# Performance work log

Hardware: AMD Instinct MI355X
Metric: run time of the kernel (lower is better)

## Reference

```python
import jax, jax.numpy as jnp
import numpy as np

K = 5
BN_EPS = 1e-5


def _knn(xyz1, xyz2, embedding_lens):
    # squared pairwise distances [B, N, S]
    d2 = (jnp.sum(xyz1 ** 2, -1)[:, :, None]
          + jnp.sum(xyz2 ** 2, -1)[:, None, :]
          - 2.0 * jnp.einsum('bnc,bsc->bns', xyz1, xyz2))
    S = xyz2.shape[1]
    valid2 = jnp.arange(S)[None, :] < embedding_lens[:, None]  # [B, S]
    d2 = jnp.where(valid2[:, None, :], d2, jnp.float32(1e10))
    neg, idx = jax.lax.top_k(-d2, K)  # K smallest distances
    return -neg, idx  # squared dists [B,N,K], indices [B,N,K]


def _masked_bn(x, mask_f, gamma, beta):
    # x: [B, N, C]; mask_f: [B, N, 1] float; stats over valid positions only
    cnt = jnp.sum(mask_f)
    mean = jnp.sum(x * mask_f, axis=(0, 1)) / cnt
    var = jnp.sum(((x - mean) ** 2) * mask_f, axis=(0, 1)) / cnt
    return (x - mean) * jax.lax.rsqrt(var + BN_EPS) * gamma + beta


def setup_inputs() -> dict:
    key = jax.random.key(0)
    ks = jax.random.split(key, 8)
    B, N, S, D1, D2 = 16, 2048, 512, 384, 384
    xyz1 = jax.random.normal(ks[0], (B, N, 3), jnp.float32)
    xyz2 = jax.random.normal(ks[1], (B, S, 3), jnp.float32)
    points1 = jax.random.normal(ks[2], (B, N, D1), jnp.float32)
    points2 = jax.random.normal(ks[3], (B, S, D2), jnp.float32)
    point_lens = jax.random.randint(ks[4], (B,), N // 2, N + 1).astype(jnp.int32)
    embedding_lens = jax.random.randint(ks[5], (B,), S // 2, S + 1).astype(jnp.int32)
    point_mask = jnp.arange(N)[None, :] < point_lens[:, None]  # [B, N] bool
    Cin = D1 + D2
    W0 = jax.random.normal(ks[6], (768, Cin), jnp.float32) * (1.0 / np.sqrt(Cin))
    W1 = jax.random.normal(ks[7], (384, 768), jnp.float32) * (1.0 / np.sqrt(768))
    return dict(xyz1=xyz1, xyz2=xyz2, points1=points1, points2=points2,
                point_lens=point_lens, embedding_lens=embedding_lens,
                point_mask=point_mask,
                W0=W0, g0=jnp.ones((768,), jnp.float32), b0=jnp.zeros((768,), jnp.float32),
                W1=W1, g1=jnp.ones((384,), jnp.float32), b1=jnp.zeros((384,), jnp.float32))


def reference(xyz1, xyz2, points1, points2, point_lens, embedding_lens,
              point_mask, W0, g0, b0, W1, g1, b1):
    B, N, _ = xyz1.shape
    D2 = points2.shape[-1]
    dists, idx = _knn(xyz1[..., :3], xyz2, embedding_lens)
    eps = jnp.finfo(dists.dtype).eps
    dist_recip = 1.0 / (dists + eps)                    # [B, N, K]
    weight = dist_recip / jnp.sum(dist_recip, axis=2, keepdims=True)
    # masked gather: points2[b, idx[b,n,k], :] -> [B, N, K, D2]
    gathered = jnp.take_along_axis(points2, idx.reshape(B, N * K)[..., None],
                                   axis=1).reshape(B, N, K, D2)
    interp = jnp.sum(gathered * weight[..., None], axis=2)  # [B, N, D2]
    x = jnp.concatenate([points1, interp], axis=-1)          # [B, N, D1+D2]
    mask_f = point_mask.astype(x.dtype)[..., None]           # [B, N, 1]
    for W, g, b in ((W0, g0, b0), (W1, g1, b1)):
        x = jnp.einsum('bnc,dc->bnd', x, W)  # 1x1 conv, no bias
        x = jax.nn.relu(_masked_bn(x, mask_f, g, b))
    return x
```

## Files before the change

### kernel.cpp

```cpp
#include <hip/hip_runtime.h>
#include <cstdint>
#include <cstddef>

typedef unsigned short u16;
typedef __bf16 bf16x8 __attribute__((ext_vector_type(8)));
typedef float    f32x4 __attribute__((ext_vector_type(4)));
typedef unsigned int u32x4 __attribute__((ext_vector_type(4)));

constexpr int BB   = 16;
constexpr int NN   = 2048;
constexpr int SS   = 512;
constexpr int DD   = 384;
constexpr int CIN  = 768;
constexpr int HID  = 768;
constexpr int OUTC = 384;
constexpr int MROWS = BB * NN;
constexpr float KNN_EPS = 1.1920929e-07f;
constexpr float BN_EPS  = 1e-5f;

constexpr size_t OFF_W0B  = 0;
constexpr size_t OFF_W1B  = OFF_W0B  + (size_t)HID*CIN*2;
constexpr size_t OFF_IDX  = OFF_W1B  + (size_t)OUTC*HID*2;
constexpr size_t OFF_WGT  = OFF_IDX  + (size_t)MROWS*5*4;
constexpr size_t OFF_SUM1 = OFF_WGT  + (size_t)MROWS*5*4;
constexpr size_t OFF_SUM2 = OFF_SUM1 + (size_t)HID*2*4;
constexpr size_t OFF_COEF1= OFF_SUM2 + (size_t)OUTC*2*4;
constexpr size_t OFF_COEF2= OFF_COEF1+ (size_t)HID*2*4;
constexpr size_t OFF_XCAT = OFF_COEF2+ (size_t)OUTC*2*4;
constexpr size_t OFF_H1   = OFF_XCAT + (size_t)MROWS*CIN*2;

__device__ inline float bf2f(u16 u){ unsigned int i = ((unsigned int)u)<<16; float f; __builtin_memcpy(&f,&i,4); return f; }
__device__ inline u16 f2bf(float f){ unsigned int x; __builtin_memcpy(&x,&f,4);
  unsigned int r = (x + 0x7fffu + ((x>>16)&1u)) >> 16; return (u16)r; }

__device__ inline void async16(const void* g, void* l){
  __builtin_amdgcn_global_load_lds((const __attribute__((address_space(1))) void*)g,
                                   (__attribute__((address_space(3))) void*)l, 16, 0, 0);
}

__global__ void cvtw_kernel(const float* __restrict__ W0, const float* __restrict__ W1,
                            u16* __restrict__ W0b, u16* __restrict__ W1b){
  int t = blockIdx.x*256 + threadIdx.x;
  if (t < HID*CIN)  W0b[t] = f2bf(W0[t]);
  if (t < OUTC*HID) W1b[t] = f2bf(W1[t]);
}

__global__ __launch_bounds__(256) void knn_kernel(const float* __restrict__ xyz1,
                                                  const float* __restrict__ xyz2,
                                                  const int* __restrict__ elens,
                                                  int* __restrict__ idxO, float* __restrict__ wO){
  __shared__ f32x4 sp[SS];
  const int tid = threadIdx.x;
  const int wv = tid >> 6, lane = tid & 63;
  const int wg = blockIdx.x*4 + wv;
  const int b = wg >> 11;
  const int n = wg & (NN-1);
  for (int s = tid; s < SS; s += 256){
    float x = xyz2[((size_t)b*SS + s)*3 + 0];
    float y = xyz2[((size_t)b*SS + s)*3 + 1];
    float z = xyz2[((size_t)b*SS + s)*3 + 2];
    f32x4 v; v[0]=x; v[1]=y; v[2]=z; v[3]=x*x+y*y+z*z;
    sp[s]=v;
  }
  __syncthreads();
  const size_t qoff = ((size_t)b*NN + n)*3;
  const float qx = xyz1[qoff+0], qy = xyz1[qoff+1], qz = xyz1[qoff+2];
  const float qq = qx*qx + qy*qy + qz*qz;
  const int Sl = elens[b];

  float d0=1e30f,d1=1e30f,d2v=1e30f,d3=1e30f,d4=1e30f;
  int   i0=0,i1=0,i2=0,i3=0,i4=0;
  #pragma unroll
  for (int j=0;j<8;j++){
    const int s = lane + j*64;
    f32x4 v = sp[s];
    float d = (s < Sl) ? (qq + v[3] - 2.f*(qx*v[0] + qy*v[1] + qz*v[2])) : 1e30f;
    bool lt4=d<d4, lt3=d<d3, lt2=d<d2v, lt1=d<d1, lt0=d<d0;
    float nd4 = lt3 ? d3 : (lt4 ? d : d4); int ni4 = lt3 ? i3 : (lt4 ? s : i4);
    float nd3 = lt2 ? d2v: (lt3 ? d : d3); int ni3 = lt2 ? i2 : (lt3 ? s : i3);
    float nd2 = lt1 ? d1 : (lt2 ? d : d2v);int ni2 = lt1 ? i1 : (lt2 ? s : i2);
    float nd1 = lt0 ? d0 : (lt1 ? d : d1); int ni1 = lt0 ? i0 : (lt1 ? s : i1);
    float nd0 = lt0 ? d  : d0;             int ni0 = lt0 ? s  : i0;
    d4=nd4;i4=ni4; d3=nd3;i3=ni3; d2v=nd2;i2=ni2; d1=nd1;i1=ni1; d0=nd0;i0=ni0;
  }
  float outd[5]; int outi[5];
  #pragma unroll
  for (int r=0;r<5;r++){
    float bd = d0; int bs = i0;
    #pragma unroll
    for (int m=1;m<64;m<<=1){
      float od = __shfl_xor(bd, m, 64);
      int   os = __shfl_xor(bs, m, 64);
      if (od < bd || (od == bd && os < bs)){ bd = od; bs = os; }
    }
    outd[r]=bd; outi[r]=bs;
    if (d0 == bd && i0 == bs){ d0=d1;i0=i1; d1=d2v;i1=i2; d2v=d3;i2=i3; d3=d4;i3=i4; d4=1e30f;i4=0; }
  }
  if (lane == 0){
    float r0=1.f/(outd[0]+KNN_EPS), r1=1.f/(outd[1]+KNN_EPS), r2=1.f/(outd[2]+KNN_EPS),
          r3=1.f/(outd[3]+KNN_EPS), r4=1.f/(outd[4]+KNN_EPS);
    float inv = 1.f/(r0+r1+r2+r3+r4);
    size_t base = (size_t)wg*5;
    idxO[base+0]=outi[0]; idxO[base+1]=outi[1]; idxO[base+2]=outi[2]; idxO[base+3]=outi[3]; idxO[base+4]=outi[4];
    wO[base+0]=r0*inv; wO[base+1]=r1*inv; wO[base+2]=r2*inv; wO[base+3]=r3*inv; wO[base+4]=r4*inv;
  }
}

__global__ __launch_bounds__(384) void xcat_kernel(const float* __restrict__ p1,
                                                   const float* __restrict__ p2,
                                                   const int* __restrict__ idx,
                                                   const float* __restrict__ wgt,
                                                   u16* __restrict__ xcat){
  const int c = threadIdx.x;
  const int rowbase = blockIdx.x*8;
  for (int i=0;i<8;i++){
    const int row = rowbase + i;
    const int b = row >> 11;
    float v1 = p1[(size_t)row*DD + c];
    xcat[(size_t)row*CIN + c] = f2bf(v1);
    float acc = 0.f;
    size_t ib = (size_t)row*5;
    #pragma unroll
    for (int k=0;k<5;k++){
      int id = idx[ib+k]; float w = wgt[ib+k];
      acc += w * p2[((size_t)b*SS + id)*DD + c];
    }
    xcat[(size_t)row*CIN + DD + c] = f2bf(acc);
  }
}

template<bool OUT_BF16, bool FUSE_A, int GX, int K>
__global__ __launch_bounds__(256) void gemm_kernel(const u16* __restrict__ A,
                                                   const u16* __restrict__ Bw,
                                                   void* __restrict__ Cout,
                                                   const int* __restrict__ plen,
                                                   float* __restrict__ sums,
                                                   const float* __restrict__ cf){
  constexpr int NC = GX*128;
  constexpr int NSTEP = K/32;
  constexpr int NWG = GX*256;
  constexpr int CPX = NWG/8;
  constexpr int NAB = FUSE_A ? 2 : 3;
  __shared__ u16 As[NAB][128*32];
  __shared__ u16 Bs[3][128*32];
  const int tid  = threadIdx.x;
  const int lane = tid & 63, wv = tid >> 6;
  const int wr = wv >> 1, wc = wv & 1;
  const int l15 = lane & 15, l16 = lane >> 4;
  const int sw  = (l15 >> 1) & 3;

  const int logical = (blockIdx.x & 7)*CPX + (blockIdx.x >> 3);
  const int bn = logical % GX, bm = logical / GX;

  int c8S[2], ldso[2];
  const u16* Ab[2]; const u16* Bb[2];
  #pragma unroll
  for (int j=0;j<2;j++){
    int ch = j*256 + wv*64 + lane;
    int row = ch >> 2;
    int c8 = (ch & 3) ^ ((ch >> 3) & 3);
    c8S[j] = c8;
    ldso[j] = (j*256 + wv*64)*16;
    Ab[j] = A  + (size_t)(bm*128 + row)*K + c8*8;
    Bb[j] = Bw + (size_t)(bn*128 + row)*K + c8*8;
  }

  auto stageA = [&](int nb, int kt){
    #pragma unroll
    for (int j=0;j<2;j++) async16(Ab[j] + kt*32, (char*)&As[nb][0] + ldso[j]);
  };
  auto stageB = [&](int nb, int kt){
    #pragma unroll
    for (int j=0;j<2;j++) async16(Bb[j] + kt*32, (char*)&Bs[nb][0] + ldso[j]);
  };
  u32x4 hv0, hv1;
  auto loadA = [&](int kt){
    hv0 = *reinterpret_cast<const u32x4*>(Ab[0] + kt*32);
    hv1 = *reinterpret_cast<const u32x4*>(Ab[1] + kt*32);
  };
  auto bnwrite = [&](int nb, int kt){
    #pragma unroll
    for (int j=0;j<2;j++){
      const int k0 = kt*32 + c8S[j]*8;
      float av[8], bv[8];
      *reinterpret_cast<f32x4*>(av)   = *reinterpret_cast<const f32x4*>(cf + k0);
      *reinterpret_cast<f32x4*>(av+4) = *reinterpret_cast<const f32x4*>(cf + k0 + 4);
      *reinterpret_cast<f32x4*>(bv)   = *reinterpret_cast<const f32x4*>(cf + K + k0);
      *reinterpret_cast<f32x4*>(bv+4) = *reinterpret_cast<const f32x4*>(cf + K + k0 + 4);
      u32x4 v = j ? hv1 : hv0; u32x4 o;
      #pragma unroll
      for (int q=0;q<4;q++){
        float lo = bf2f((u16)(v[q] & 0xffffu));
        float hi = bf2f((u16)(v[q] >> 16));
        lo = fmaxf(lo*av[2*q]   + bv[2*q],   0.f);
        hi = fmaxf(hi*av[2*q+1] + bv[2*q+1], 0.f);
        o[q] = (unsigned int)f2bf(lo) | ((unsigned int)f2bf(hi) << 16);
      }
      *reinterpret_cast<u32x4*>((char*)&As[nb][0] + ldso[j] + lane*16) = o;
    }
  };

  f32x4 acc[4][4] = {};

  if constexpr (FUSE_A){
    loadA(0);
    __builtin_amdgcn_sched_barrier(0);
    stageB(0, 0); stageB(1, 1);
    bnwrite(0, 0);
    asm volatile("s_waitcnt vmcnt(2) lgkmcnt(0)" ::: "memory");
    __builtin_amdgcn_s_barrier();
  } else {
    stageA(0, 0); stageB(0, 0);
    stageA(1, 1); stageB(1, 1);
    asm volatile("s_waitcnt vmcnt(4) lgkmcnt(0)" ::: "memory");
    __builtin_amdgcn_s_barrier();
  }

  int rb = 0, wb = 2;
  for (int kt=0; kt<NSTEP; ++kt){
    const bool pf1 = (kt+1 < NSTEP), pf2 = (kt+2 < NSTEP);
    if constexpr (FUSE_A){
      if (pf1) loadA(kt+1);
      __builtin_amdgcn_sched_barrier(0);
      if (pf2) stageB(wb, kt+2);
    } else {
      if (pf2){ stageA(wb, kt+2); stageB(wb, kt+2); }
    }

    bf16x8 af[4], bfr[4];
    const int aslot = FUSE_A ? (kt & 1) : rb;
    #pragma unroll
    for (int m=0;m<4;m++){
      int r = wr*64 + m*16 + l15;
      af[m] = *reinterpret_cast<const bf16x8*>(&As[aslot][r*32 + ((l16 ^ sw) << 3)]);
    }
    #pragma unroll
    for (int n=0;n<4;n++){
      int c = wc*64 + n*16 + l15;
      bfr[n] = *reinterpret_cast<const bf16x8*>(&Bs[rb][c*32 + ((l16 ^ sw) << 3)]);
    }
    #pragma unroll
    for (int m=0;m<4;m++)
      #pragma unroll
      for (int n=0;n<4;n++)
        acc[m][n] = __builtin_amdgcn_mfma_f32_16x16x32_bf16(af[m], bfr[n], acc[m][n], 0, 0, 0);

    if constexpr (FUSE_A){ if (pf1) bnwrite((kt+1)&1, kt+1); }

    if (pf1){
      if (pf2){
        if constexpr (FUSE_A) asm volatile("s_waitcnt vmcnt(2) lgkmcnt(0)" ::: "memory");
        else                  asm volatile("s_waitcnt vmcnt(4) lgkmcnt(0)" ::: "memory");
      } else {
        asm volatile("s_waitcnt vmcnt(0) lgkmcnt(0)" ::: "memory");
      }
      __builtin_amdgcn_s_barrier();
    }
    rb = (rb==2) ? 0 : rb+1;
    wb = (wb==2) ? 0 : wb+1;
  }

  #pragma unroll
  for (int m=0;m<4;m++){
    int r0 = bm*128 + wr*64 + m*16 + l16*4;
    #pragma unroll
    for (int n=0;n<4;n++){
      int c = bn*128 + wc*64 + n*16 + l15;
      #pragma unroll
      for (int r=0;r<4;r++){
        size_t off = (size_t)(r0+r)*NC + c;
        if (OUT_BF16) ((u16*)Cout)[off] = f2bf(acc[m][n][r]);
        else          ((float*)Cout)[off] = acc[m][n][r];
      }
    }
  }

  const int pl = plen[bm >> 4];
  const int rbase = (bm & 15)*128 + wr*64 + l16*4;
  float cs[4] = {0.f,0.f,0.f,0.f}, cs2[4] = {0.f,0.f,0.f,0.f};
  #pragma unroll
  for (int m=0;m<4;m++){
    #pragma unroll
    for (int r=0;r<4;r++){
      if (rbase + m*16 + r < pl){
        #pragma unroll
        for (int n=0;n<4;n++){
          float v = acc[m][n][r];
          cs[n] += v; cs2[n] += v*v;
        }
      }
    }
  }
  #pragma unroll
  for (int n=0;n<4;n++){
    cs[n]  += __shfl_xor(cs[n], 16, 64);  cs[n]  += __shfl_xor(cs[n], 32, 64);
    cs2[n] += __shfl_xor(cs2[n], 16, 64); cs2[n] += __shfl_xor(cs2[n], 32, 64);
  }
  float* lsum = (float*)&As[0][0];
  lsum[tid] = 0.f;
  __syncthreads();
  if (l16 == 0){
    #pragma unroll
    for (int n=0;n<4;n++){
      int col = wc*64 + n*16 + l15;
      atomicAdd(&lsum[col], cs[n]);
      atomicAdd(&lsum[128 + col], cs2[n]);
    }
  }
  __syncthreads();
  if (tid < 128)       atomicAdd(&sums[bn*128 + tid], lsum[tid]);
  else                 atomicAdd(&sums[NC + bn*128 + (tid-128)], lsum[tid]);
}

__global__ void coef_kernel(const float* __restrict__ sums, const int* __restrict__ plen,
                            const float* __restrict__ g, const float* __restrict__ bta,
                            float* __restrict__ coef, int C){
  int c = threadIdx.x;
  if (c >= C) return;
  float cnt = 0.f;
  for (int b=0;b<BB;b++) cnt += (float)plen[b];
  float mean = sums[c] / cnt;
  float var  = sums[C + c] / cnt - mean*mean;
  var = fmaxf(var, 0.f);
  float a = g[c] * rsqrtf(var + BN_EPS);
  coef[c] = a;
  coef[C + c] = bta[c] - mean*a;
}

__global__ __launch_bounds__(256) void final_kernel(float* __restrict__ Y,
                                                    const float* __restrict__ coef){
  size_t t = (size_t)blockIdx.x*256 + threadIdx.x;
  size_t f = t*4;
  int c = (int)(f % (size_t)OUTC);
  f32x4 v = *reinterpret_cast<const f32x4*>(Y + f);
  #pragma unroll
  for (int j=0;j<4;j++)
    v[j] = fmaxf(v[j]*coef[c+j] + coef[OUTC+c+j], 0.f);
  *reinterpret_cast<f32x4*>(Y + f) = v;
}

extern "C" void kernel_launch(void* const* d_in, const int* in_sizes, int n_in,
                              void* d_out, int out_size, void* d_ws, size_t ws_size,
                              hipStream_t stream){
  (void)in_sizes; (void)n_in; (void)out_size; (void)ws_size;
  const float* xyz1 = (const float*)d_in[0];
  const float* xyz2 = (const float*)d_in[1];
  const float* p1   = (const float*)d_in[2];
  const float* p2   = (const float*)d_in[3];
  const int*   plen = (const int*)d_in[4];
  const int*   elen = (const int*)d_in[5];
  const float* W0   = (const float*)d_in[7];
  const float* g0   = (const float*)d_in[8];
  const float* b0   = (const float*)d_in[9];
  const float* W1   = (const float*)d_in[10];
  const float* g1   = (const float*)d_in[11];
  const float* b1   = (const float*)d_in[12];
  float* out = (float*)d_out;
  char*  ws  = (char*)d_ws;

  u16*   W0b  = (u16*)  (ws + OFF_W0B);
  u16*   W1b  = (u16*)  (ws + OFF_W1B);
  int*   idxb = (int*)  (ws + OFF_IDX);
  float* wgtb = (float*)(ws + OFF_WGT);
  float* sum1 = (float*)(ws + OFF_SUM1);
  float* sum2 = (float*)(ws + OFF_SUM2);
  float* coef1= (float*)(ws + OFF_COEF1);
  float* coef2= (float*)(ws + OFF_COEF2);
  u16*   xcat = (u16*)  (ws + OFF_XCAT);
  u16*   h1   = (u16*)  (ws + OFF_H1);

  hipMemsetAsync(ws + OFF_SUM1, 0, (size_t)(HID*2 + OUTC*2)*4, stream);

  cvtw_kernel<<<(HID*CIN + 255)/256, 256, 0, stream>>>(W0, W1, W0b, W1b);
  knn_kernel<<<MROWS/4, 256, 0, stream>>>(xyz1, xyz2, elen, idxb, wgtb);
  xcat_kernel<<<MROWS/8, 384, 0, stream>>>(p1, p2, idxb, wgtb, xcat);

  gemm_kernel<true, false, 6, CIN><<<6*256, 256, 0, stream>>>(xcat, W0b, h1, plen, sum1, nullptr);
  coef_kernel<<<1, HID, 0, stream>>>(sum1, plen, g0, b0, coef1, HID);

  gemm_kernel<false, true, 3, HID><<<3*256, 256, 0, stream>>>(h1, W1b, out, plen, sum2, coef1);
  coef_kernel<<<1, OUTC, 0, stream>>>(sum2, plen, g1, b1, coef2, OUTC);
  final_kernel<<<(size_t)MROWS*OUTC/4/256, 256, 0, stream>>>(out, coef2);
}
```

Baseline: 193.4 us.

## Split first GEMM into 512-thread double-buffered kernel and vectorize xcat gather

The first GEMM becomes a dedicated kernel with 8 waves per block (each owning a 64x32 sub-tile) and double-buffered LDS. It interleaves async staging of A and B between split halves of the MFMA work and raises wave priority around the MFMAs, aiming to hide load latency better. The xcat gather kernel now uses float4 loads and processes 4 rows per block instead of looping over 8 rows with scalar accesses. The second GEMM is de-templated with unchanged logic. The extra barriers per k-step add synchronization cost, and each wave now reuses its loaded fragments across fewer MFMAs.

```diff
diff --git a/kernel.cpp b/kernel.cpp
--- a/kernel.cpp
+++ b/kernel.cpp
@@ -6,6 +6,7 @@
 typedef __bf16 bf16x8 __attribute__((ext_vector_type(8)));
 typedef float    f32x4 __attribute__((ext_vector_type(4)));
 typedef unsigned int u32x4 __attribute__((ext_vector_type(4)));
+typedef unsigned short u16x4 __attribute__((ext_vector_type(4)));
 
 constexpr int BB   = 16;
 constexpr int NN   = 2048;
@@ -111,37 +112,185 @@
                                                    const int* __restrict__ idx,
                                                    const float* __restrict__ wgt,
                                                    u16* __restrict__ xcat){
-  const int c = threadIdx.x;
-  const int rowbase = blockIdx.x*8;
-  for (int i=0;i<8;i++){
-    const int row = rowbase + i;
-    const int b = row >> 11;
-    float v1 = p1[(size_t)row*DD + c];
-    xcat[(size_t)row*CIN + c] = f2bf(v1);
-    float acc = 0.f;
-    size_t ib = (size_t)row*5;
-    #pragma unroll
-    for (int k=0;k<5;k++){
-      int id = idx[ib+k]; float w = wgt[ib+k];
-      acc += w * p2[((size_t)b*SS + id)*DD + c];
-    }
-    xcat[(size_t)row*CIN + DD + c] = f2bf(acc);
-  }
-}
-
-template<bool OUT_BF16, bool FUSE_A, int GX, int K>
-__global__ __launch_bounds__(256) void gemm_kernel(const u16* __restrict__ A,
-                                                   const u16* __restrict__ Bw,
-                                                   void* __restrict__ Cout,
-                                                   const int* __restrict__ plen,
-                                                   float* __restrict__ sums,
-                                                   const float* __restrict__ cf){
+  const int t = threadIdx.x;
+  const int rloc = t / 96, c4 = t % 96;
+  const int row = blockIdx.x*4 + rloc;
+  const int b = row >> 11;
+  const int c = c4*4;
+  f32x4 v1 = *reinterpret_cast<const f32x4*>(p1 + (size_t)row*DD + c);
+  size_t ib = (size_t)row*5;
+  f32x4 acc = {0.f,0.f,0.f,0.f};
+  #pragma unroll
+  for (int k=0;k<5;k++){
+    int id = idx[ib+k]; float w = wgt[ib+k];
+    f32x4 g = *reinterpret_cast<const f32x4*>(p2 + ((size_t)b*SS + id)*DD + c);
+    #pragma unroll
+    for (int j=0;j<4;j++) acc[j] += w * g[j];
+  }
+  u16x4 o1, o2;
+  #pragma unroll
+  for (int j=0;j<4;j++){ o1[j] = f2bf(v1[j]); o2[j] = f2bf(acc[j]); }
+  *reinterpret_cast<u16x4*>(xcat + (size_t)row*CIN + c)      = o1;
+  *reinterpret_cast<u16x4*>(xcat + (size_t)row*CIN + DD + c) = o2;
+}
+
+__global__ __launch_bounds__(512, 6) void gemm1_kernel(const u16* __restrict__ A,
+                                                       const u16* __restrict__ Bw,
+                                                       u16* __restrict__ Cout,
+                                                       const int* __restrict__ plen,
+                                                       float* __restrict__ sums){
+  constexpr int K   = CIN;
+  constexpr int NC  = HID;
+  constexpr int GX  = NC/128;
+  constexpr int NT  = K/32;
+  constexpr int NWG = GX*256;
+  constexpr int CPX = NWG/8;
+  __shared__ u16 Ash[2][128*32];
+  __shared__ u16 Bsh[2][128*32];
+  const int tid  = threadIdx.x;
+  const int lane = tid & 63, wv = tid >> 6;
+  const int wr = wv >> 2, wc = wv & 3;
+  const int l15 = lane & 15, l16 = lane >> 4;
+  const int swz = (l15 >> 1) & 3;
+
+  const int logical = (blockIdx.x & 7)*CPX + (blockIdx.x >> 3);
+  const int bn = logical % GX, bm = logical / GX;
+
+  const int srow = tid >> 2;
+  const int sk4  = (tid & 3) ^ ((tid >> 3) & 3);
+  const u16* gA = A  + (size_t)(bm*128 + srow)*K + sk4*8;
+  const u16* gB = Bw + (size_t)(bn*128 + srow)*K + sk4*8;
+  const int dst = (wv*64)*16;
+
+  auto stageA = [&](int tt, int bi){ async16(gA + tt*32, (char*)&Ash[bi][0] + dst); };
+  auto stageB = [&](int tt, int bi){ async16(gB + tt*32, (char*)&Bsh[bi][0] + dst); };
+
+  int aoff[4], boff[2];
+  #pragma unroll
+  for (int m=0;m<4;m++) aoff[m] = (wr*64 + m*16 + l15)*32 + ((l16 ^ swz) << 3);
+  #pragma unroll
+  for (int n=0;n<2;n++) boff[n] = (wc*32 + n*16 + l15)*32 + ((l16 ^ swz) << 3);
+
+  f32x4 acc[4][2] = {};
+
+  stageA(0,0); stageB(0,0); stageA(1,1); stageB(1,1);
+  asm volatile("s_waitcnt vmcnt(2)" ::: "memory");
+  __builtin_amdgcn_s_barrier();
+  __builtin_amdgcn_sched_barrier(0);
+
+  for (int t=0; t<NT; ++t){
+    const int cur = t & 1;
+    const int tt = (t+2 < NT) ? (t+2) : (NT-1);
+    bf16x8 af0 = *reinterpret_cast<const bf16x8*>(&Ash[cur][aoff[0]]);
+    bf16x8 af1 = *reinterpret_cast<const bf16x8*>(&Ash[cur][aoff[1]]);
+    bf16x8 af2 = *reinterpret_cast<const bf16x8*>(&Ash[cur][aoff[2]]);
+    bf16x8 af3 = *reinterpret_cast<const bf16x8*>(&Ash[cur][aoff[3]]);
+    bf16x8 bv0 = *reinterpret_cast<const bf16x8*>(&Bsh[cur][boff[0]]);
+    asm volatile("s_waitcnt lgkmcnt(0)" ::: "memory");
+    __builtin_amdgcn_s_barrier();
+    __builtin_amdgcn_sched_barrier(0);
+    stageA(tt, cur);
+    __builtin_amdgcn_s_setprio(1);
+    acc[0][0] = __builtin_amdgcn_mfma_f32_16x16x32_bf16(af0, bv0, acc[0][0], 0,0,0);
+    acc[1][0] = __builtin_amdgcn_mfma_f32_16x16x32_bf16(af1, bv0, acc[1][0], 0,0,0);
+    acc[2][0] = __builtin_amdgcn_mfma_f32_16x16x32_bf16(af2, bv0, acc[2][0], 0,0,0);
+    acc[3][0] = __builtin_amdgcn_mfma_f32_16x16x32_bf16(af3, bv0, acc[3][0], 0,0,0);
+    __builtin_amdgcn_s_setprio(0);
+    bf16x8 bv1 = *reinterpret_cast<const bf16x8*>(&Bsh[cur][boff[1]]);
+    asm volatile("s_waitcnt lgkmcnt(0)" ::: "memory");
+    __builtin_amdgcn_s_barrier();
+    __builtin_amdgcn_sched_barrier(0);
+    stageB(tt, cur);
+    __builtin_amdgcn_s_setprio(1);
+    acc[0][1] = __builtin_amdgcn_mfma_f32_16x16x32_bf16(af0, bv1, acc[0][1], 0,0,0);
+    acc[1][1] = __builtin_amdgcn_mfma_f32_16x16x32_bf16(af1, bv1, acc[1][1], 0,0,0);
+    acc[2][1] = __builtin_amdgcn_mfma_f32_16x16x32_bf16(af2, bv1, acc[2][1], 0,0,0);
+    acc[3][1] = __builtin_amdgcn_mfma_f32_16x16x32_bf16(af3, bv1, acc[3][1], 0,0,0);
+    __builtin_amdgcn_s_setprio(0);
+    asm volatile("s_waitcnt vmcnt(2)" ::: "memory");
+    __builtin_amdgcn_s_barrier();
+    __builtin_amdgcn_sched_barrier(0);
+  }
+  asm volatile("s_waitcnt vmcnt(0)" ::: "memory");
+  __syncthreads();
+
+  #pragma unroll
+  for (int m=0;m<4;m++){
+    int r0 = bm*128 + wr*64 + m*16 + l16*4;
+    #pragma unroll
+    for (int n=0;n<2;n++){
+      int c = bn*128 + wc*32 + n*16 + l15;
+      #pragma unroll
+      for (int r=0;r<4;r++)
+        Cout[(size_t)(r0+r)*NC + c] = f2bf(acc[m][n][r]);
+    }
+  }
+
+  const int pl = plen[bm >> 4];
+  const int rbase = (bm & 15)*128 + wr*64 + l16*4;
+  float cs[2] = {0.f,0.f}, cs2[2] = {0.f,0.f};
+  #pragma unroll
+  for (int m=0;m<4;m++){
+    #pragma unroll
+    for (int r=0;r<4;r++){
+      if (rbase + m*16 + r < pl){
+        #pragma unroll
+        for (int n=0;n<2;n++){
+          float v = acc[m][n][r];
+          cs[n] += v; cs2[n] += v*v;
+        }
+      }
+    }
+  }
+  #pragma unroll
+  for (int n=0;n<2;n++){
+    cs[n]  += __shfl_xor(cs[n], 16, 64);  cs[n]  += __shfl_xor(cs[n], 32, 64);
+    cs2[n] += __shfl_xor(cs2[n], 16, 64); cs2[n] += __shfl_xor(cs2[n], 32, 64);
+  }
+  float* lsum = (float*)&Ash[0][0];
+  if (tid < 256) lsum[tid] = 0.f;
+  __syncthreads();
+  if (l16 == 0){
+    #pragma unroll
+    for (int n=0;n<2;n++){
+      int col = wc*32 + n*16 + l15;
+      atomicAdd(&lsum[col], cs[n]);
+      atomicAdd(&lsum[128 + col], cs2[n]);
+    }
+  }
+  __syncthreads();
+  if (tid < 128)       atomicAdd(&sums[bn*128 + tid], lsum[tid]);
+  else if (tid < 256)  atomicAdd(&sums[NC + bn*128 + (tid-128)], lsum[tid]);
+}
+
+__global__ void coef_kernel(const float* __restrict__ sums, const int* __restrict__ plen,
+                            const float* __restrict__ g, const float* __restrict__ bta,
+                            float* __restrict__ coef, int C){
+  int c = threadIdx.x;
+  if (c >= C) return;
+  float cnt = 0.f;
+  for (int b=0;b<BB;b++) cnt += (float)plen[b];
+  float mean = sums[c] / cnt;
+  float var  = sums[C + c] / cnt - mean*mean;
+  var = fmaxf(var, 0.f);
+  float a = g[c] * rsqrtf(var + BN_EPS);
+  coef[c] = a;
+  coef[C + c] = bta[c] - mean*a;
+}
+
+__global__ __launch_bounds__(256) void gemm2_kernel(const u16* __restrict__ A,
+                                                    const u16* __restrict__ Bw,
+                                                    float* __restrict__ Cout,
+                                                    const int* __restrict__ plen,
+                                                    float* __restrict__ sums,
+                                                    const float* __restrict__ cf){
+  constexpr int GX = 3;
+  constexpr int K  = HID;
   constexpr int NC = GX*128;
   constexpr int NSTEP = K/32;
   constexpr int NWG = GX*256;
   constexpr int CPX = NWG/8;
-  constexpr int NAB = FUSE_A ? 2 : 3;
-  __shared__ u16 As[NAB][128*32];
+  __shared__ u16 As[2][128*32];
   __shared__ u16 Bs[3][128*32];
   const int tid  = threadIdx.x;
   const int lane = tid & 63, wv = tid >> 6;
@@ -165,10 +314,6 @@
     Bb[j] = Bw + (size_t)(bn*128 + row)*K + c8*8;
   }
 
-  auto stageA = [&](int nb, int kt){
-    #pragma unroll
-    for (int j=0;j<2;j++) async16(Ab[j] + kt*32, (char*)&As[nb][0] + ldso[j]);
-  };
   auto stageB = [&](int nb, int kt){
     #pragma unroll
     for (int j=0;j<2;j++) async16(Bb[j] + kt*32, (char*)&Bs[nb][0] + ldso[j]);
@@ -202,33 +347,22 @@
 
   f32x4 acc[4][4] = {};
 
-  if constexpr (FUSE_A){
-    loadA(0);
-    __builtin_amdgcn_sched_barrier(0);
-    stageB(0, 0); stageB(1, 1);
-    bnwrite(0, 0);
-    asm volatile("s_waitcnt vmcnt(2) lgkmcnt(0)" ::: "memory");
-    __builtin_amdgcn_s_barrier();
-  } else {
-    stageA(0, 0); stageB(0, 0);
-    stageA(1, 1); stageB(1, 1);
-    asm volatile("s_waitcnt vmcnt(4) lgkmcnt(0)" ::: "memory");
-    __builtin_amdgcn_s_barrier();
-  }
+  loadA(0);
+  __builtin_amdgcn_sched_barrier(0);
+  stageB(0, 0); stageB(1, 1);
+  bnwrite(0, 0);
+  asm volatile("s_waitcnt vmcnt(2) lgkmcnt(0)" ::: "memory");
+  __builtin_amdgcn_s_barrier();
 
   int rb = 0, wb = 2;
   for (int kt=0; kt<NSTEP; ++kt){
     const bool pf1 = (kt+1 < NSTEP), pf2 = (kt+2 < NSTEP);
-    if constexpr (FUSE_A){
-      if (pf1) loadA(kt+1);
-      __builtin_amdgcn_sched_barrier(0);
-      if (pf2) stageB(wb, kt+2);
-    } else {
-      if (pf2){ stageA(wb, kt+2); stageB(wb, kt+2); }
-    }
+    if (pf1) loadA(kt+1);
+    __builtin_amdgcn_sched_barrier(0);
+    if (pf2) stageB(wb, kt+2);
 
     bf16x8 af[4], bfr[4];
-    const int aslot = FUSE_A ? (kt & 1) : rb;
+    const int aslot = kt & 1;
     #pragma unroll
     for (int m=0;m<4;m++){
       int r = wr*64 + m*16 + l15;
@@ -245,15 +379,11 @@
       for (int n=0;n<4;n++)
         acc[m][n] = __builtin_amdgcn_mfma_f32_16x16x32_bf16(af[m], bfr[n], acc[m][n], 0, 0, 0);
 
-    if constexpr (FUSE_A){ if (pf1) bnwrite((kt+1)&1, kt+1); }
+    if (pf1) bnwrite((kt+1)&1, kt+1);
 
     if (pf1){
-      if (pf2){
-        if constexpr (FUSE_A) asm volatile("s_waitcnt vmcnt(2) lgkmcnt(0)" ::: "memory");
-        else                  asm volatile("s_waitcnt vmcnt(4) lgkmcnt(0)" ::: "memory");
-      } else {
-        asm volatile("s_waitcnt vmcnt(0) lgkmcnt(0)" ::: "memory");
-      }
+      if (pf2) asm volatile("s_waitcnt vmcnt(2) lgkmcnt(0)" ::: "memory");
+      else     asm volatile("s_waitcnt vmcnt(0) lgkmcnt(0)" ::: "memory");
       __builtin_amdgcn_s_barrier();
     }
     rb = (rb==2) ? 0 : rb+1;
@@ -267,11 +397,8 @@
     for (int n=0;n<4;n++){
       int c = bn*128 + wc*64 + n*16 + l15;
       #pragma unroll
-      for (int r=0;r<4;r++){
-        size_t off = (size_t)(r0+r)*NC + c;
-        if (OUT_BF16) ((u16*)Cout)[off] = f2bf(acc[m][n][r]);
-        else          ((float*)Cout)[off] = acc[m][n][r];
-      }
+      for (int r=0;r<4;r++)
+        Cout[(size_t)(r0+r)*NC + c] = acc[m][n][r];
     }
   }
 
@@ -310,21 +437,6 @@
   __syncthreads();
   if (tid < 128)       atomicAdd(&sums[bn*128 + tid], lsum[tid]);
   else                 atomicAdd(&sums[NC + bn*128 + (tid-128)], lsum[tid]);
-}
-
-__global__ void coef_kernel(const float* __restrict__ sums, const int* __restrict__ plen,
-                            const float* __restrict__ g, const float* __restrict__ bta,
-                            float* __restrict__ coef, int C){
-  int c = threadIdx.x;
-  if (c >= C) return;
-  float cnt = 0.f;
-  for (int b=0;b<BB;b++) cnt += (float)plen[b];
-  float mean = sums[c] / cnt;
-  float var  = sums[C + c] / cnt - mean*mean;
-  var = fmaxf(var, 0.f);
-  float a = g[c] * rsqrtf(var + BN_EPS);
-  coef[c] = a;
-  coef[C + c] = bta[c] - mean*a;
 }
 
 __global__ __launch_bounds__(256) void final_kernel(float* __restrict__ Y,
@@ -373,12 +485,12 @@
 
   cvtw_kernel<<<(HID*CIN + 255)/256, 256, 0, stream>>>(W0, W1, W0b, W1b);
   knn_kernel<<<MROWS/4, 256, 0, stream>>>(xyz1, xyz2, elen, idxb, wgtb);
-  xcat_kernel<<<MROWS/8, 384, 0, stream>>>(p1, p2, idxb, wgtb, xcat);
-
-  gemm_kernel<true, false, 6, CIN><<<6*256, 256, 0, stream>>>(xcat, W0b, h1, plen, sum1, nullptr);
+  xcat_kernel<<<MROWS/4, 384, 0, stream>>>(p1, p2, idxb, wgtb, xcat);
+
+  gemm1_kernel<<<6*256, 512, 0, stream>>>(xcat, W0b, h1, plen, sum1);
   coef_kernel<<<1, HID, 0, stream>>>(sum1, plen, g0, b0, coef1, HID);
 
-  gemm_kernel<false, true, 3, HID><<<3*256, 256, 0, stream>>>(h1, W1b, out, plen, sum2, coef1);
+  gemm2_kernel<<<3*256, 256, 0, stream>>>(h1, W1b, out, plen, sum2, coef1);
   coef_kernel<<<1, OUTC, 0, stream>>>(sum2, plen, g1, b1, coef2, OUTC);
   final_kernel<<<(size_t)MROWS*OUTC/4/256, 256, 0, stream>>>(out, coef2);
 }
```

New measurement: 187.4 us. -3.1%, faster.
